# Kernel tuning notes

Measured on AMD Instinct MI355X. Metric: run time of the kernel, lower is better.

## Reference

```python
import jax, jax.numpy as jnp
import numpy as np

M, N, V, E = 128, 1024, 32000, 512  # seq_len, batch, vocab, embedding/hidden


def setup_inputs() -> dict:
    key = jax.random.key(0)
    k0, k1, k2, k3, k4, k5 = jax.random.split(key, 6)
    s = 1.0 / np.sqrt(E)  # GRUCell default init scale
    return {
        "utterance": jax.random.randint(k0, (M, N), 0, V, dtype=jnp.int32),
        "emb_table": jax.random.normal(k1, (V, E), dtype=jnp.float32),
        "W_ih": jax.random.normal(k2, (3 * E, E), dtype=jnp.float32) * s,
        "W_hh": jax.random.normal(k3, (3 * E, E), dtype=jnp.float32) * s,
        "b_ih": jax.random.normal(k4, (3 * E,), dtype=jnp.float32) * s,
        "b_hh": jax.random.normal(k5, (3 * E,), dtype=jnp.float32) * s,
        "term_id": 0,
    }


def reference(utterance, emb_table, W_ih, W_hh, b_ih, b_hh, term_id):
    # Equivalent to the alive-sieve loop: each row's state freezes AFTER the
    # step where its token == term_id (that step is still processed).
    n_batch = utterance.shape[1]
    e = emb_table.shape[1]

    def step(carry, tok):
        state, alive = carry                       # [N,E], [N] bool
        emb = emb_table[tok]                       # [N,E] gather
        gi = emb @ W_ih.T + b_ih                   # [N,3E]
        gh = state @ W_hh.T + b_hh                 # [N,3E]
        i_r, i_z, i_n = jnp.split(gi, 3, axis=-1)
        h_r, h_z, h_n = jnp.split(gh, 3, axis=-1)
        r = jax.nn.sigmoid(i_r + h_r)
        z = jax.nn.sigmoid(i_z + h_z)
        n = jnp.tanh(i_n + r * h_n)
        new_state = (1.0 - z) * n + z * state
        state = jnp.where(alive[:, None], new_state, state)
        alive = alive & (tok != term_id)
        return (state, alive), None

    init = (jnp.zeros((n_batch, e), dtype=emb_table.dtype),
            jnp.ones((n_batch,), dtype=bool))
    (final_state, _), _ = jax.lax.scan(step, init, utterance)
    return final_state  # [N,E]
```

## Files before the change

### kernel.cpp

```cpp
#include <hip/hip_runtime.h>
#include <stdint.h>
#include <stddef.h>

#define MSTEPS 128
#define NB 1024
#define ED 512
#define GD 1536
#define VS 32000

#define RB 32
#define CB 64
#define NRB 32
#define NCB 8
#define GIST 200
#define STST 80

typedef __attribute__((ext_vector_type(4))) float f32x4;
typedef __attribute__((ext_vector_type(8))) short s16x8;
typedef __attribute__((ext_vector_type(4))) short s16x4;
typedef __attribute__((ext_vector_type(8))) unsigned short u16x8;

__device__ __forceinline__ unsigned short f2bf(float f) {
  unsigned x = __builtin_bit_cast(unsigned, f);
  x = x + 0x7fffu + ((x >> 16) & 1u);
  return (unsigned short)(x >> 16);
}
__device__ __forceinline__ float bf2f(unsigned short u) {
  return __builtin_bit_cast(float, ((unsigned)u) << 16);
}
__device__ __forceinline__ float sigm(float x) { return 1.0f / (1.0f + __expf(-x)); }
__device__ __forceinline__ float tanh_(float x) {
  x = fminf(15.0f, fmaxf(-15.0f, x));
  float e = __expf(-2.0f * x);
  return (1.0f - e) / (1.0f + e);
}

__global__ __launch_bounds__(256) void table_kernel(
    const float* __restrict__ emb, const float* __restrict__ Wih,
    const float* __restrict__ bih, unsigned short* __restrict__ tab)
{
  __shared__ short Al[128 * 64];
  __shared__ short Bl[128 * 64];
  const int tid = threadIdx.x;
  const int lane = tid & 63;
  const int l15 = lane & 15, l4 = lane >> 4;
  const int wv = tid >> 6;
  const int rh = wv & 1, ch = wv >> 1;
  const int row0 = blockIdx.x * 128;
  const int col0 = blockIdx.y * 128;

  f32x4 acc[4][4];
  #pragma unroll
  for (int m = 0; m < 4; m++)
    #pragma unroll
    for (int n = 0; n < 4; n++) acc[m][n] = (f32x4){0.f, 0.f, 0.f, 0.f};

  for (int ko = 0; ko < ED; ko += 64) {
    #pragma unroll
    for (int i = 0; i < 8; i++) {
      int idx = tid + i * 256;
      int r = idx >> 4, c4 = idx & 15;
      int ba = (r * 128 + c4 * 8) ^ ((r & 7) << 4);
      f32x4 va = *(const f32x4*)(emb + (size_t)(row0 + r) * ED + ko + c4 * 4);
      s16x4 pa;
      pa[0] = (short)f2bf(va[0]); pa[1] = (short)f2bf(va[1]);
      pa[2] = (short)f2bf(va[2]); pa[3] = (short)f2bf(va[3]);
      *(s16x4*)((char*)Al + ba) = pa;
      f32x4 vb = *(const f32x4*)(Wih + (size_t)(col0 + r) * ED + ko + c4 * 4);
      s16x4 pb;
      pb[0] = (short)f2bf(vb[0]); pb[1] = (short)f2bf(vb[1]);
      pb[2] = (short)f2bf(vb[2]); pb[3] = (short)f2bf(vb[3]);
      *(s16x4*)((char*)Bl + ba) = pb;
    }
    __syncthreads();
    #pragma unroll
    for (int kk = 0; kk < 2; kk++) {
      s16x8 af[4], bfv[4];
      #pragma unroll
      for (int m = 0; m < 4; m++) {
        int row = rh * 64 + m * 16 + l15;
        int ad = (row * 128 + kk * 64 + l4 * 16) ^ ((row & 7) << 4);
        af[m] = *(const s16x8*)((char*)Al + ad);
      }
      #pragma unroll
      for (int n = 0; n < 4; n++) {
        int col = ch * 64 + n * 16 + l15;
        int ad = (col * 128 + kk * 64 + l4 * 16) ^ ((col & 7) << 4);
        bfv[n] = *(const s16x8*)((char*)Bl + ad);
      }
      #pragma unroll
      for (int m = 0; m < 4; m++)
        #pragma unroll
        for (int n = 0; n < 4; n++)
          acc[m][n] = __builtin_amdgcn_mfma_f32_16x16x32_bf16(af[m], bfv[n], acc[m][n], 0, 0, 0);
    }
    __syncthreads();
  }

  float bias_n[4];
  #pragma unroll
  for (int n = 0; n < 4; n++) bias_n[n] = bih[col0 + ch * 64 + n * 16 + l15];
  #pragma unroll
  for (int m = 0; m < 4; m++)
    #pragma unroll
    for (int n = 0; n < 4; n++) {
      int colg = col0 + ch * 64 + n * 16 + l15;
      #pragma unroll
      for (int j = 0; j < 4; j++) {
        int rowg = row0 + rh * 64 + m * 16 + l4 * 4 + j;
        tab[(size_t)rowg * GD + colg] = f2bf(acc[m][n][j] + bias_n[n]);
      }
    }
}

__global__ __launch_bounds__(256, 1) void gru_kernel(
    const int* __restrict__ utt, const float* __restrict__ Whh,
    const float* __restrict__ bhh, const unsigned short* __restrict__ tab,
    unsigned short* st0, unsigned short* st1,
    unsigned* cnt, int* abort_g, const int* __restrict__ termp,
    float* __restrict__ out)
{
  __shared__ __align__(16) char sls[RB * 1024];
  __shared__ __align__(16) unsigned short gil[RB * GIST];
  __shared__ __align__(16) unsigned short stl[RB * STST];
  __shared__ int abl;

  const int tid = threadIdx.x;
  const int lane = tid & 63;
  const int l15 = lane & 15, l4 = lane >> 4;
  const int wv = tid >> 6;
  const int bid = blockIdx.x;
  const int rblk = bid & (NRB - 1), cblk = bid >> 5;
  const int r0 = rblk * RB, c0 = cblk * CB;
  const int wc = wv * 16 + l15;
  const int termid = termp[0];
  unsigned* cnt_r = cnt + rblk * 32;
  const int grow = tid >> 3, gq = tid & 7;

  s16x8 bfr[3][16];
  #pragma unroll
  for (int g = 0; g < 3; g++)
    #pragma unroll
    for (int kk = 0; kk < 16; kk++) {
      const float* src = Whh + (size_t)(g * ED + c0 + wc) * ED + kk * 32 + l4 * 8;
      f32x4 v0 = *(const f32x4*)(src);
      f32x4 v1 = *(const f32x4*)(src + 4);
      s16x8 p;
      p[0] = (short)f2bf(v0[0]); p[1] = (short)f2bf(v0[1]);
      p[2] = (short)f2bf(v0[2]); p[3] = (short)f2bf(v0[3]);
      p[4] = (short)f2bf(v1[0]); p[5] = (short)f2bf(v1[1]);
      p[6] = (short)f2bf(v1[2]); p[7] = (short)f2bf(v1[3]);
      bfr[g][kk] = p;
    }

  float bh[3];
  #pragma unroll
  for (int g = 0; g < 3; g++) bh[g] = bhh[g * ED + c0 + wc];

  float ms[2][4] = {{0.f, 0.f, 0.f, 0.f}, {0.f, 0.f, 0.f, 0.f}};
  unsigned am = 0xFFu;

  u16x8 pg0, pg1, pg2;
  int ptoks[8];
  {
    int tok = utt[r0 + grow];
    const unsigned short* tb = tab + (size_t)tok * GD + c0 + gq * 8;
    pg0 = *(const u16x8*)(tb);
    pg1 = *(const u16x8*)(tb + ED);
    pg2 = *(const u16x8*)(tb + 2 * ED);
    #pragma unroll
    for (int a = 0; a < 2; a++)
      #pragma unroll
      for (int j = 0; j < 4; j++)
        ptoks[a * 4 + j] = utt[r0 + a * 16 + l4 * 4 + j];
  }

  for (int s = 0; s < MSTEPS; s++) {
    const unsigned short* rdb = (s & 1) ? st1 : st0;
    unsigned short* wrb = (s & 1) ? st0 : st1;

    unsigned long long sld[16];
    const unsigned long long* sb = (const unsigned long long*)(rdb + (size_t)r0 * ED);
    #pragma unroll
    for (int i = 0; i < 16; i++)
      sld[i] = __hip_atomic_load(sb + i * 256 + tid, __ATOMIC_RELAXED, __HIP_MEMORY_SCOPE_AGENT);

    {
      char* gb = (char*)gil + grow * (GIST * 2) + gq * 16;
      *(u16x8*)(gb + 0 * 128) = pg0;
      *(u16x8*)(gb + 1 * 128) = pg1;
      *(u16x8*)(gb + 2 * 128) = pg2;
    }
    int tk[8];
    #pragma unroll
    for (int i = 0; i < 8; i++) tk[i] = ptoks[i];

    #pragma unroll
    for (int i = 0; i < 16; i++) {
      int o = i * 2048 + tid * 8;
      int row = o >> 10;
      *(unsigned long long*)(sls + (o ^ ((row & 7) << 4))) = sld[i];
    }
    __syncthreads();

    if (s + 1 < MSTEPS) {
      int tok = utt[(s + 1) * NB + r0 + grow];
      const unsigned short* tb = tab + (size_t)tok * GD + c0 + gq * 8;
      pg0 = *(const u16x8*)(tb);
      pg1 = *(const u16x8*)(tb + ED);
      pg2 = *(const u16x8*)(tb + 2 * ED);
      #pragma unroll
      for (int a = 0; a < 2; a++)
        #pragma unroll
        for (int j = 0; j < 4; j++)
          ptoks[a * 4 + j] = utt[(s + 1) * NB + r0 + a * 16 + l4 * 4 + j];
    }

    f32x4 acc[2][3];
    #pragma unroll
    for (int a = 0; a < 2; a++)
      #pragma unroll
      for (int g = 0; g < 3; g++) acc[a][g] = (f32x4){0.f, 0.f, 0.f, 0.f};
    #pragma unroll
    for (int kk = 0; kk < 16; kk++) {
      s16x8 av[2];
      #pragma unroll
      for (int a = 0; a < 2; a++) {
        int row = a * 16 + l15;
        int ad = (row * 1024 + kk * 64 + l4 * 16) ^ ((row & 7) << 4);
        av[a] = *(const s16x8*)(sls + ad);
      }
      #pragma unroll
      for (int a = 0; a < 2; a++)
        #pragma unroll
        for (int g = 0; g < 3; g++)
          acc[a][g] = __builtin_amdgcn_mfma_f32_16x16x32_bf16(av[a], bfr[g][kk], acc[a][g], 0, 0, 0);
    }

    #pragma unroll
    for (int a = 0; a < 2; a++) {
      #pragma unroll
      for (int j = 0; j < 4; j++) {
        int row = a * 16 + l4 * 4 + j;
        float hr = acc[a][0][j] + bh[0];
        float hz = acc[a][1][j] + bh[1];
        float hn = acc[a][2][j] + bh[2];
        float ir = bf2f(gil[row * GIST + 0 * 64 + wc]);
        float iz = bf2f(gil[row * GIST + 1 * 64 + wc]);
        float in_ = bf2f(gil[row * GIST + 2 * 64 + wc]);
        float r = sigm(ir + hr);
        float z = sigm(iz + hz);
        float nn = tanh_(in_ + r * hn);
        float old = ms[a][j];
        float nu = (1.0f - z) * nn + z * old;
        float res = ((am >> (a * 4 + j)) & 1u) ? nu : old;
        ms[a][j] = res;
        stl[row * STST + wc] = f2bf(res);
        if (tk[a * 4 + j] == termid) am &= ~(1u << (a * 4 + j));
      }
    }
    __syncthreads();

    {
      union { u16x8 v; unsigned long long u[2]; } cv;
      cv.v = *(const u16x8*)(stl + grow * STST + gq * 8);
      unsigned long long* dst =
          (unsigned long long*)(wrb + (size_t)(r0 + grow) * ED + c0 + gq * 8);
      __hip_atomic_store(dst, cv.u[0], __ATOMIC_RELAXED, __HIP_MEMORY_SCOPE_AGENT);
      __hip_atomic_store(dst + 1, cv.u[1], __ATOMIC_RELAXED, __HIP_MEMORY_SCOPE_AGENT);
    }

    asm volatile("s_waitcnt vmcnt(0)" ::: "memory");
    __syncthreads();
    if (tid == 0) {
      __hip_atomic_fetch_add(cnt_r, 1u, __ATOMIC_RELEASE, __HIP_MEMORY_SCOPE_AGENT);
      unsigned target = (unsigned)NCB * (unsigned)(s + 1);
      unsigned long long t0 = __builtin_amdgcn_s_memrealtime();
      int ab = 0, pc = 0;
      while (__hip_atomic_load(cnt_r, __ATOMIC_RELAXED, __HIP_MEMORY_SCOPE_AGENT) < target) {
        if (((++pc) & 63) == 0) {
          if (__hip_atomic_load(abort_g, __ATOMIC_RELAXED, __HIP_MEMORY_SCOPE_AGENT)) { ab = 1; break; }
          if (__builtin_amdgcn_s_memrealtime() - t0 > 20000000ULL) {
            __hip_atomic_store(abort_g, 1, __ATOMIC_RELAXED, __HIP_MEMORY_SCOPE_AGENT);
            ab = 1; break;
          }
        }
      }
      abl = ab;
    }
    __syncthreads();
    if (abl) break;
  }

  #pragma unroll
  for (int a = 0; a < 2; a++)
    #pragma unroll
    for (int j = 0; j < 4; j++) {
      int n = r0 + a * 16 + l4 * 4 + j;
      out[(size_t)n * ED + c0 + wc] = ms[a][j];
    }
}

__global__ void fail_kernel(float* out) {
  if (threadIdx.x == 0 && blockIdx.x == 0) out[0] = -54321.0f;
}

extern "C" void kernel_launch(void* const* d_in, const int* in_sizes, int n_in,
                              void* d_out, int out_size, void* d_ws, size_t ws_size,
                              hipStream_t stream) {
  const int* utt = (const int*)d_in[0];
  const float* emb = (const float*)d_in[1];
  const float* Wih = (const float*)d_in[2];
  const float* Whh = (const float*)d_in[3];
  const float* bih = (const float*)d_in[4];
  const float* bhh = (const float*)d_in[5];
  const int* term = (const int*)d_in[6];
  float* out = (float*)d_out;
  char* ws = (char*)d_ws;

  const size_t tab_b = (size_t)VS * GD * 2;
  const size_t st_b = (size_t)NB * ED * 2;
  const size_t off_st0 = tab_b;
  const size_t off_st1 = off_st0 + st_b;
  const size_t off_cnt = off_st1 + st_b;
  const size_t need = off_cnt + 8192;

  if (ws_size < need) {
    fail_kernel<<<1, 64, 0, stream>>>(out);
    return;
  }

  unsigned short* tab = (unsigned short*)(ws);
  unsigned short* st0 = (unsigned short*)(ws + off_st0);
  unsigned short* st1 = (unsigned short*)(ws + off_st1);
  unsigned* cnt = (unsigned*)(ws + off_cnt);
  int* abort_g = (int*)(ws + off_cnt + 6144);

  (void)hipMemsetAsync(st0, 0, st_b, stream);
  (void)hipMemsetAsync(cnt, 0, 8192, stream);

  table_kernel<<<dim3(250, 12), 256, 0, stream>>>(emb, Wih, bih, tab);
  gru_kernel<<<256, 256, 0, stream>>>(utt, Whh, bhh, tab, st0, st1,
                                      cnt, abort_g, term, out);
}
```

Measured before the change: 942.1 us.

## Repartition GRU blocks into 16-row groups with 4-way column split

Repartitions the persistent GRU kernel so each block handles 16 batch rows and 128 hidden columns with 512 threads. The per-step barrier then spans 4 blocks instead of 8. The state buffer ring grows from 2 to 4 slots, and the zero initial state is handled by skipping the matmul at step 0 instead of a memset. Token ids are now read inside each step rather than prefetched. Smaller sync groups should cut spin-wait latency, but each block now holds 8 waves with full W_hh fragments, and launch_bounds(512,2) may force register spills.

```diff
diff --git a/kernel.cpp b/kernel.cpp
--- a/kernel.cpp
+++ b/kernel.cpp
@@ -8,12 +8,12 @@
 #define GD 1536
 #define VS 32000
 
-#define RB 32
-#define CB 64
-#define NRB 32
-#define NCB 8
-#define GIST 200
-#define STST 80
+#define RB 16
+#define CB 128
+#define NGR 64
+#define NSH 4
+#define GIST 392
+#define STST 136
 
 typedef __attribute__((ext_vector_type(4))) float f32x4;
 typedef __attribute__((ext_vector_type(8))) short s16x8;
@@ -113,11 +113,10 @@
     }
 }
 
-__global__ __launch_bounds__(256, 1) void gru_kernel(
+__global__ __launch_bounds__(512, 2) void gru_kernel(
     const int* __restrict__ utt, const float* __restrict__ Whh,
     const float* __restrict__ bhh, const unsigned short* __restrict__ tab,
-    unsigned short* st0, unsigned short* st1,
-    unsigned* cnt, int* abort_g, const int* __restrict__ termp,
+    unsigned short* st, unsigned* cnt, const int* __restrict__ termp,
     float* __restrict__ out)
 {
   __shared__ __align__(16) char sls[RB * 1024];
@@ -130,12 +129,14 @@
   const int l15 = lane & 15, l4 = lane >> 4;
   const int wv = tid >> 6;
   const int bid = blockIdx.x;
-  const int rblk = bid & (NRB - 1), cblk = bid >> 5;
+  const int rblk = bid & (NGR - 1);
+  const int cblk = bid >> 6;
   const int r0 = rblk * RB, c0 = cblk * CB;
   const int wc = wv * 16 + l15;
   const int termid = termp[0];
+
   unsigned* cnt_r = cnt + rblk * 32;
-  const int grow = tid >> 3, gq = tid & 7;
+  int* abort_g = (int*)(cnt + 2048);
 
   s16x8 bfr[3][16];
   #pragma unroll
@@ -157,124 +158,110 @@
   #pragma unroll
   for (int g = 0; g < 3; g++) bh[g] = bhh[g * ED + c0 + wc];
 
-  float ms[2][4] = {{0.f, 0.f, 0.f, 0.f}, {0.f, 0.f, 0.f, 0.f}};
-  unsigned am = 0xFFu;
-
-  u16x8 pg0, pg1, pg2;
-  int ptoks[8];
+  float ms[4] = {0.f, 0.f, 0.f, 0.f};
+  unsigned am = 0xFu;
+
+  const int u0 = tid, u1 = 512 + tid;
+  const int r0u0 = u0 / 48, sg0 = u0 % 48;
+  const int r0u1 = u1 / 48, sg1 = u1 % 48;
+
+  u16x8 pgA, pgB;
   {
-    int tok = utt[r0 + grow];
-    const unsigned short* tb = tab + (size_t)tok * GD + c0 + gq * 8;
-    pg0 = *(const u16x8*)(tb);
-    pg1 = *(const u16x8*)(tb + ED);
-    pg2 = *(const u16x8*)(tb + 2 * ED);
-    #pragma unroll
-    for (int a = 0; a < 2; a++)
-      #pragma unroll
-      for (int j = 0; j < 4; j++)
-        ptoks[a * 4 + j] = utt[r0 + a * 16 + l4 * 4 + j];
+    int tokA = utt[r0 + r0u0];
+    pgA = *(const u16x8*)(tab + (size_t)tokA * GD + (sg0 >> 4) * ED + c0 + (sg0 & 15) * 8);
+    if (tid < 256) {
+      int tokB = utt[r0 + r0u1];
+      pgB = *(const u16x8*)(tab + (size_t)tokB * GD + (sg1 >> 4) * ED + c0 + (sg1 & 15) * 8);
+    }
   }
 
   for (int s = 0; s < MSTEPS; s++) {
-    const unsigned short* rdb = (s & 1) ? st1 : st0;
-    unsigned short* wrb = (s & 1) ? st0 : st1;
-
-    unsigned long long sld[16];
-    const unsigned long long* sb = (const unsigned long long*)(rdb + (size_t)r0 * ED);
-    #pragma unroll
-    for (int i = 0; i < 16; i++)
-      sld[i] = __hip_atomic_load(sb + i * 256 + tid, __ATOMIC_RELAXED, __HIP_MEMORY_SCOPE_AGENT);
-
-    {
-      char* gb = (char*)gil + grow * (GIST * 2) + gq * 16;
-      *(u16x8*)(gb + 0 * 128) = pg0;
-      *(u16x8*)(gb + 1 * 128) = pg1;
-      *(u16x8*)(gb + 2 * 128) = pg2;
-    }
-    int tk[8];
-    #pragma unroll
-    for (int i = 0; i < 8; i++) tk[i] = ptoks[i];
-
-    #pragma unroll
-    for (int i = 0; i < 16; i++) {
-      int o = i * 2048 + tid * 8;
-      int row = o >> 10;
-      *(unsigned long long*)(sls + (o ^ ((row & 7) << 4))) = sld[i];
+    const unsigned short* rdb = st + (size_t)((s + 3) & 3) * NB * ED;
+    unsigned short* wrb = st + (size_t)(s & 3) * NB * ED;
+
+    unsigned long long sld[4];
+    if (s > 0) {
+      const unsigned long long* sb = (const unsigned long long*)(rdb + (size_t)r0 * ED);
+      #pragma unroll
+      for (int k = 0; k < 4; k++)
+        sld[k] = __hip_atomic_load(sb + k * 512 + tid, __ATOMIC_RELAXED, __HIP_MEMORY_SCOPE_AGENT);
+    }
+
+    *(u16x8*)(gil + r0u0 * GIST + (sg0 >> 4) * 128 + (sg0 & 15) * 8) = pgA;
+    if (tid < 256)
+      *(u16x8*)(gil + r0u1 * GIST + (sg1 >> 4) * 128 + (sg1 & 15) * 8) = pgB;
+    int tk[4];
+    #pragma unroll
+    for (int j = 0; j < 4; j++) tk[j] = utt[s * NB + r0 + l4 * 4 + j];
+
+    if (s > 0) {
+      #pragma unroll
+      for (int k = 0; k < 4; k++) {
+        int i = k * 512 + tid;
+        int row = i >> 7;
+        int o = row * 1024 + (i & 127) * 8;
+        *(unsigned long long*)(sls + (o ^ ((row & 7) << 4))) = sld[k];
+      }
     }
     __syncthreads();
 
     if (s + 1 < MSTEPS) {
-      int tok = utt[(s + 1) * NB + r0 + grow];
-      const unsigned short* tb = tab + (size_t)tok * GD + c0 + gq * 8;
-      pg0 = *(const u16x8*)(tb);
-      pg1 = *(const u16x8*)(tb + ED);
-      pg2 = *(const u16x8*)(tb + 2 * ED);
-      #pragma unroll
-      for (int a = 0; a < 2; a++)
-        #pragma unroll
-        for (int j = 0; j < 4; j++)
-          ptoks[a * 4 + j] = utt[(s + 1) * NB + r0 + a * 16 + l4 * 4 + j];
-    }
-
-    f32x4 acc[2][3];
-    #pragma unroll
-    for (int a = 0; a < 2; a++)
-      #pragma unroll
-      for (int g = 0; g < 3; g++) acc[a][g] = (f32x4){0.f, 0.f, 0.f, 0.f};
-    #pragma unroll
-    for (int kk = 0; kk < 16; kk++) {
-      s16x8 av[2];
-      #pragma unroll
-      for (int a = 0; a < 2; a++) {
-        int row = a * 16 + l15;
-        int ad = (row * 1024 + kk * 64 + l4 * 16) ^ ((row & 7) << 4);
-        av[a] = *(const s16x8*)(sls + ad);
-      }
-      #pragma unroll
-      for (int a = 0; a < 2; a++)
+      int tokA = utt[(s + 1) * NB + r0 + r0u0];
+      pgA = *(const u16x8*)(tab + (size_t)tokA * GD + (sg0 >> 4) * ED + c0 + (sg0 & 15) * 8);
+      if (tid < 256) {
+        int tokB = utt[(s + 1) * NB + r0 + r0u1];
+        pgB = *(const u16x8*)(tab + (size_t)tokB * GD + (sg1 >> 4) * ED + c0 + (sg1 & 15) * 8);
+      }
+    }
+
+    f32x4 acc[3];
+    #pragma unroll
+    for (int g = 0; g < 3; g++) acc[g] = (f32x4){0.f, 0.f, 0.f, 0.f};
+    if (s > 0) {
+      #pragma unroll
+      for (int kk = 0; kk < 16; kk++) {
+        int ad = (l15 * 1024 + kk * 64 + l4 * 16) ^ ((l15 & 7) << 4);
+        s16x8 av = *(const s16x8*)(sls + ad);
         #pragma unroll
         for (int g = 0; g < 3; g++)
-          acc[a][g] = __builtin_amdgcn_mfma_f32_16x16x32_bf16(av[a], bfr[g][kk], acc[a][g], 0, 0, 0);
-    }
-
-    #pragma unroll
-    for (int a = 0; a < 2; a++) {
-      #pragma unroll
-      for (int j = 0; j < 4; j++) {
-        int row = a * 16 + l4 * 4 + j;
-        float hr = acc[a][0][j] + bh[0];
-        float hz = acc[a][1][j] + bh[1];
-        float hn = acc[a][2][j] + bh[2];
-        float ir = bf2f(gil[row * GIST + 0 * 64 + wc]);
-        float iz = bf2f(gil[row * GIST + 1 * 64 + wc]);
-        float in_ = bf2f(gil[row * GIST + 2 * 64 + wc]);
-        float r = sigm(ir + hr);
-        float z = sigm(iz + hz);
-        float nn = tanh_(in_ + r * hn);
-        float old = ms[a][j];
-        float nu = (1.0f - z) * nn + z * old;
-        float res = ((am >> (a * 4 + j)) & 1u) ? nu : old;
-        ms[a][j] = res;
-        stl[row * STST + wc] = f2bf(res);
-        if (tk[a * 4 + j] == termid) am &= ~(1u << (a * 4 + j));
-      }
+          acc[g] = __builtin_amdgcn_mfma_f32_16x16x32_bf16(av, bfr[g][kk], acc[g], 0, 0, 0);
+      }
+    }
+
+    #pragma unroll
+    for (int j = 0; j < 4; j++) {
+      int row = l4 * 4 + j;
+      float hr = acc[0][j] + bh[0];
+      float hz = acc[1][j] + bh[1];
+      float hn = acc[2][j] + bh[2];
+      float ir = bf2f(gil[row * GIST + 0 * 128 + wc]);
+      float iz = bf2f(gil[row * GIST + 1 * 128 + wc]);
+      float in_ = bf2f(gil[row * GIST + 2 * 128 + wc]);
+      float r = sigm(ir + hr);
+      float z = sigm(iz + hz);
+      float nn = tanh_(in_ + r * hn);
+      float old = ms[j];
+      float nu = (1.0f - z) * nn + z * old;
+      float res = ((am >> j) & 1u) ? nu : old;
+      ms[j] = res;
+      stl[row * STST + wc] = f2bf(res);
+      if (tk[j] == termid) am &= ~(1u << j);
     }
     __syncthreads();
 
     {
-      union { u16x8 v; unsigned long long u[2]; } cv;
-      cv.v = *(const u16x8*)(stl + grow * STST + gq * 8);
+      int srow = tid >> 5, sseg = tid & 31;
+      unsigned long long v = *(const unsigned long long*)(stl + srow * STST + sseg * 4);
       unsigned long long* dst =
-          (unsigned long long*)(wrb + (size_t)(r0 + grow) * ED + c0 + gq * 8);
-      __hip_atomic_store(dst, cv.u[0], __ATOMIC_RELAXED, __HIP_MEMORY_SCOPE_AGENT);
-      __hip_atomic_store(dst + 1, cv.u[1], __ATOMIC_RELAXED, __HIP_MEMORY_SCOPE_AGENT);
+          (unsigned long long*)(wrb + (size_t)(r0 + srow) * ED + c0 + sseg * 4);
+      __hip_atomic_store(dst, v, __ATOMIC_RELAXED, __HIP_MEMORY_SCOPE_AGENT);
     }
 
     asm volatile("s_waitcnt vmcnt(0)" ::: "memory");
     __syncthreads();
     if (tid == 0) {
       __hip_atomic_fetch_add(cnt_r, 1u, __ATOMIC_RELEASE, __HIP_MEMORY_SCOPE_AGENT);
-      unsigned target = (unsigned)NCB * (unsigned)(s + 1);
+      unsigned target = (unsigned)NSH * (unsigned)(s + 1);
       unsigned long long t0 = __builtin_amdgcn_s_memrealtime();
       int ab = 0, pc = 0;
       while (__hip_atomic_load(cnt_r, __ATOMIC_RELAXED, __HIP_MEMORY_SCOPE_AGENT) < target) {
@@ -293,12 +280,10 @@
   }
 
   #pragma unroll
-  for (int a = 0; a < 2; a++)
-    #pragma unroll
-    for (int j = 0; j < 4; j++) {
-      int n = r0 + a * 16 + l4 * 4 + j;
-      out[(size_t)n * ED + c0 + wc] = ms[a][j];
-    }
+  for (int j = 0; j < 4; j++) {
+    int n = r0 + l4 * 4 + j;
+    out[(size_t)n * ED + c0 + wc] = ms[j];
+  }
 }
 
 __global__ void fail_kernel(float* out) {
@@ -320,10 +305,9 @@
 
   const size_t tab_b = (size_t)VS * GD * 2;
   const size_t st_b = (size_t)NB * ED * 2;
-  const size_t off_st0 = tab_b;
-  const size_t off_st1 = off_st0 + st_b;
-  const size_t off_cnt = off_st1 + st_b;
-  const size_t need = off_cnt + 8192;
+  const size_t off_st = tab_b;
+  const size_t off_cnt = off_st + 4 * st_b;
+  const size_t need = off_cnt + 16384;
 
   if (ws_size < need) {
     fail_kernel<<<1, 64, 0, stream>>>(out);
@@ -331,15 +315,11 @@
   }
 
   unsigned short* tab = (unsigned short*)(ws);
-  unsigned short* st0 = (unsigned short*)(ws + off_st0);
-  unsigned short* st1 = (unsigned short*)(ws + off_st1);
+  unsigned short* st = (unsigned short*)(ws + off_st);
   unsigned* cnt = (unsigned*)(ws + off_cnt);
-  int* abort_g = (int*)(ws + off_cnt + 6144);
-
-  (void)hipMemsetAsync(st0, 0, st_b, stream);
-  (void)hipMemsetAsync(cnt, 0, 8192, stream);
+
+  (void)hipMemsetAsync(cnt, 0, 16384, stream);
 
   table_kernel<<<dim3(250, 12), 256, 0, stream>>>(emb, Wih, bih, tab);
-  gru_kernel<<<256, 256, 0, stream>>>(utt, Whh, bhh, tab, st0, st1,
-                                      cnt, abort_g, term, out);
-}
+  gru_kernel<<<256, 512, 0, stream>>>(utt, Whh, bhh, tab, st, cnt, term, out);
+}
```

Result: slower. 1.788 ms (+89.8%).

## Replace per-row-group atomic counter barrier with per-block flags; skip step-zero matmul

Applied to the files above, without the earlier changes.

The inter-block barrier used to have each column block atomically increment a shared counter and poll it. It now has each block store its step number into its own flag slot. Waiters read all eight flags with four 64-bit acquire loads and take the minimum, which removes read-modify-write contention on a single address. The abort check also runs more often. Separately, step zero skips the state load, the LDS staging and the recurrent MFMA because the initial state is zero, so the memset of the first state buffer is dropped as well.

```diff
diff --git a/kernel.cpp b/kernel.cpp
--- a/kernel.cpp
+++ b/kernel.cpp
@@ -117,7 +117,7 @@
     const int* __restrict__ utt, const float* __restrict__ Whh,
     const float* __restrict__ bhh, const unsigned short* __restrict__ tab,
     unsigned short* st0, unsigned short* st1,
-    unsigned* cnt, int* abort_g, const int* __restrict__ termp,
+    unsigned* cnt, const int* __restrict__ termp,
     float* __restrict__ out)
 {
   __shared__ __align__(16) char sls[RB * 1024];
@@ -134,8 +134,10 @@
   const int r0 = rblk * RB, c0 = cblk * CB;
   const int wc = wv * 16 + l15;
   const int termid = termp[0];
-  unsigned* cnt_r = cnt + rblk * 32;
   const int grow = tid >> 3, gq = tid & 7;
+
+  unsigned* fl = cnt + rblk * 16;
+  int* abort_g = (int*)(cnt + 1024);
 
   s16x8 bfr[3][16];
   #pragma unroll
@@ -180,10 +182,12 @@
     unsigned short* wrb = (s & 1) ? st0 : st1;
 
     unsigned long long sld[16];
-    const unsigned long long* sb = (const unsigned long long*)(rdb + (size_t)r0 * ED);
-    #pragma unroll
-    for (int i = 0; i < 16; i++)
-      sld[i] = __hip_atomic_load(sb + i * 256 + tid, __ATOMIC_RELAXED, __HIP_MEMORY_SCOPE_AGENT);
+    if (s > 0) {
+      const unsigned long long* sb = (const unsigned long long*)(rdb + (size_t)r0 * ED);
+      #pragma unroll
+      for (int i = 0; i < 16; i++)
+        sld[i] = __hip_atomic_load(sb + i * 256 + tid, __ATOMIC_RELAXED, __HIP_MEMORY_SCOPE_AGENT);
+    }
 
     {
       char* gb = (char*)gil + grow * (GIST * 2) + gq * 16;
@@ -195,11 +199,13 @@
     #pragma unroll
     for (int i = 0; i < 8; i++) tk[i] = ptoks[i];
 
-    #pragma unroll
-    for (int i = 0; i < 16; i++) {
-      int o = i * 2048 + tid * 8;
-      int row = o >> 10;
-      *(unsigned long long*)(sls + (o ^ ((row & 7) << 4))) = sld[i];
+    if (s > 0) {
+      #pragma unroll
+      for (int i = 0; i < 16; i++) {
+        int o = i * 2048 + tid * 8;
+        int row = o >> 10;
+        *(unsigned long long*)(sls + (o ^ ((row & 7) << 4))) = sld[i];
+      }
     }
     __syncthreads();
 
@@ -221,20 +227,22 @@
     for (int a = 0; a < 2; a++)
       #pragma unroll
       for (int g = 0; g < 3; g++) acc[a][g] = (f32x4){0.f, 0.f, 0.f, 0.f};
-    #pragma unroll
-    for (int kk = 0; kk < 16; kk++) {
-      s16x8 av[2];
-      #pragma unroll
-      for (int a = 0; a < 2; a++) {
-        int row = a * 16 + l15;
-        int ad = (row * 1024 + kk * 64 + l4 * 16) ^ ((row & 7) << 4);
-        av[a] = *(const s16x8*)(sls + ad);
-      }
-      #pragma unroll
-      for (int a = 0; a < 2; a++)
+    if (s > 0) {
+      #pragma unroll
+      for (int kk = 0; kk < 16; kk++) {
+        s16x8 av[2];
         #pragma unroll
-        for (int g = 0; g < 3; g++)
-          acc[a][g] = __builtin_amdgcn_mfma_f32_16x16x32_bf16(av[a], bfr[g][kk], acc[a][g], 0, 0, 0);
+        for (int a = 0; a < 2; a++) {
+          int row = a * 16 + l15;
+          int ad = (row * 1024 + kk * 64 + l4 * 16) ^ ((row & 7) << 4);
+          av[a] = *(const s16x8*)(sls + ad);
+        }
+        #pragma unroll
+        for (int a = 0; a < 2; a++)
+          #pragma unroll
+          for (int g = 0; g < 3; g++)
+            acc[a][g] = __builtin_amdgcn_mfma_f32_16x16x32_bf16(av[a], bfr[g][kk], acc[a][g], 0, 0, 0);
+      }
     }
 
     #pragma unroll
@@ -273,12 +281,25 @@
     asm volatile("s_waitcnt vmcnt(0)" ::: "memory");
     __syncthreads();
     if (tid == 0) {
-      __hip_atomic_fetch_add(cnt_r, 1u, __ATOMIC_RELEASE, __HIP_MEMORY_SCOPE_AGENT);
-      unsigned target = (unsigned)NCB * (unsigned)(s + 1);
+      __hip_atomic_store(fl + cblk, (unsigned)(s + 1), __ATOMIC_RELEASE, __HIP_MEMORY_SCOPE_AGENT);
+      const unsigned tgt = (unsigned)(s + 1);
       unsigned long long t0 = __builtin_amdgcn_s_memrealtime();
       int ab = 0, pc = 0;
-      while (__hip_atomic_load(cnt_r, __ATOMIC_RELAXED, __HIP_MEMORY_SCOPE_AGENT) < target) {
-        if (((++pc) & 63) == 0) {
+      for (;;) {
+        unsigned long long f01 = __hip_atomic_load((const unsigned long long*)(fl + 0), __ATOMIC_ACQUIRE, __HIP_MEMORY_SCOPE_AGENT);
+        unsigned long long f23 = __hip_atomic_load((const unsigned long long*)(fl + 2), __ATOMIC_ACQUIRE, __HIP_MEMORY_SCOPE_AGENT);
+        unsigned long long f45 = __hip_atomic_load((const unsigned long long*)(fl + 4), __ATOMIC_ACQUIRE, __HIP_MEMORY_SCOPE_AGENT);
+        unsigned long long f67 = __hip_atomic_load((const unsigned long long*)(fl + 6), __ATOMIC_ACQUIRE, __HIP_MEMORY_SCOPE_AGENT);
+        unsigned mn = (unsigned)f01;
+        mn = mn < (unsigned)(f01 >> 32) ? mn : (unsigned)(f01 >> 32);
+        mn = mn < (unsigned)f23 ? mn : (unsigned)f23;
+        mn = mn < (unsigned)(f23 >> 32) ? mn : (unsigned)(f23 >> 32);
+        mn = mn < (unsigned)f45 ? mn : (unsigned)f45;
+        mn = mn < (unsigned)(f45 >> 32) ? mn : (unsigned)(f45 >> 32);
+        mn = mn < (unsigned)f67 ? mn : (unsigned)f67;
+        mn = mn < (unsigned)(f67 >> 32) ? mn : (unsigned)(f67 >> 32);
+        if (mn >= tgt) break;
+        if (((++pc) & 15) == 0) {
           if (__hip_atomic_load(abort_g, __ATOMIC_RELAXED, __HIP_MEMORY_SCOPE_AGENT)) { ab = 1; break; }
           if (__builtin_amdgcn_s_memrealtime() - t0 > 20000000ULL) {
             __hip_atomic_store(abort_g, 1, __ATOMIC_RELAXED, __HIP_MEMORY_SCOPE_AGENT);
@@ -334,12 +355,10 @@
   unsigned short* st0 = (unsigned short*)(ws + off_st0);
   unsigned short* st1 = (unsigned short*)(ws + off_st1);
   unsigned* cnt = (unsigned*)(ws + off_cnt);
-  int* abort_g = (int*)(ws + off_cnt + 6144);
-
-  (void)hipMemsetAsync(st0, 0, st_b, stream);
+
   (void)hipMemsetAsync(cnt, 0, 8192, stream);
 
   table_kernel<<<dim3(250, 12), 256, 0, stream>>>(emb, Wih, bih, tab);
   gru_kernel<<<256, 256, 0, stream>>>(utt, Whh, bhh, tab, st0, st1,
-                                      cnt, abort_g, term, out);
-}
+                                      cnt, term, out);
+}
```

After: 2.166 ms. +129.9%, slower.
